# Kernel tuning notes

Hardware: AMD Instinct MI355X
Metric: run time of the kernel (lower is better)

## Reference

```python
import jax, jax.numpy as jnp
import numpy as np


def setup_inputs() -> dict:
    key = jax.random.key(0)
    k1, k2 = jax.random.split(key)
    B, C, H, W = 32, 8, 256, 256
    inp = jax.random.normal(k1, (B, C, H, W), dtype=jnp.float32)
    tgt = jax.random.uniform(k2, (B, C, H, W), dtype=jnp.float32)
    return {"input": inp, "target": tgt}


def reference(input, target):
    B, C, H, W = input.shape
    # normalized coordinate grids: (index+1)/size, as in the original loops
    x_grid = (jnp.arange(W, dtype=input.dtype) + 1.0) / W          # [W]
    y_grid = (jnp.arange(H, dtype=input.dtype) + 1.0) / H          # [H]

    # per-(b,c) softmax over the flattened heatmap (DSNT)
    p = jax.nn.softmax(input.reshape(B, C, H * W), axis=-1).reshape(B, C, H, W)
    pred_x = jnp.einsum('bchw,w->bc', p, x_grid)                   # [B, C]
    pred_y = jnp.einsum('bchw,h->bc', p, y_grid)                   # [B, C]

    # ground-truth coords from argmax of target heatmap
    idx = jnp.argmax(target.reshape(B, C, H * W), axis=-1)         # [B, C] int
    true_x = ((idx % W) + 1).astype(input.dtype) / W
    true_y = ((idx // W) + 1).astype(input.dtype) / H

    ed = jnp.sqrt((true_x - pred_x) ** 2 + (true_y - pred_y) ** 2)  # [B, C]
    # original sums over all (batch, channel) pairs, divides by batch size only
    return jnp.sum(ed) / B
```

## Files before the change

### kernel.cpp

```cpp
#include <hip/hip_runtime.h>
#include <math.h>


constexpr int HW    = 256 * 256;
constexpr int BLOCK = 256;
constexpr int SPLIT = 16;
constexpr int CHUNK4 = (HW / 4) / SPLIT;
constexpr int ITERS  = CHUNK4 / BLOCK;

typedef float vfloat4 __attribute__((ext_vector_type(4)));

__global__ __launch_bounds__(BLOCK, 8) void dsnt_partial_kernel(
        const float* __restrict__ input,
        const float* __restrict__ target,
        unsigned long long* __restrict__ ws_pk,
        float* __restrict__ ws_s,
        float* __restrict__ ws_sx,
        float* __restrict__ ws_sy)
{
    const int bc    = blockIdx.x >> 4;
    const int chunk = blockIdx.x & (SPLIT - 1);
    const int tid   = threadIdx.x;

    const vfloat4* __restrict__ in4 =
        reinterpret_cast<const vfloat4*>(input) + (size_t)bc * (HW / 4) + chunk * CHUNK4;
    const vfloat4* __restrict__ tg4 =
        reinterpret_cast<const vfloat4*>(target) + (size_t)bc * (HW / 4) + chunk * CHUNK4;

    float s = 0.f, sx = 0.f, sy = 0.f;
    float bv = -INFINITY;
    int   bi = 0x7FFFFFFF;

    const int fbase = 4 * chunk * CHUNK4;

    #pragma unroll
    for (int i = 0; i < ITERS; ++i) {
        const int j = tid + i * BLOCK;
        const vfloat4 v = __builtin_nontemporal_load(in4 + j);
        const vfloat4 t = tg4[j];
        const int f = fbase + 4 * j;
        const float y  = (float)((f >> 8) + 1) * (1.0f / 256.0f);
        const float x0 = (float)((f & 255) + 1) * (1.0f / 256.0f);

        const float e0 = __expf(v.x);
        const float e1 = __expf(v.y);
        const float e2 = __expf(v.z);
        const float e3 = __expf(v.w);
        const float es = (e0 + e1) + (e2 + e3);
        s  += es;
        sy += es * y;
        sx += e0 * x0
            + e1 * (x0 + 1.0f / 256.0f)
            + e2 * (x0 + 2.0f / 256.0f)
            + e3 * (x0 + 3.0f / 256.0f);

        if (t.x > bv) { bv = t.x; bi = f; }
        if (t.y > bv) { bv = t.y; bi = f + 1; }
        if (t.z > bv) { bv = t.z; bi = f + 2; }
        if (t.w > bv) { bv = t.w; bi = f + 3; }
    }

    unsigned long long pk =
        ((unsigned long long)__float_as_uint(bv) << 32) |
        (unsigned long long)(0xFFFFFFFFu - (unsigned)bi);

    #pragma unroll
    for (int off = 32; off > 0; off >>= 1) {
        s  += __shfl_down(s, off);
        sx += __shfl_down(sx, off);
        sy += __shfl_down(sy, off);
        const unsigned long long opk = __shfl_down(pk, off);
        pk = (opk > pk) ? opk : pk;
    }

    __shared__ float ls[4], lsx[4], lsy[4];
    __shared__ unsigned long long lpk[4];
    const int wave = tid >> 6;
    const int lane = tid & 63;
    if (lane == 0) {
        ls[wave]  = s;
        lsx[wave] = sx;
        lsy[wave] = sy;
        lpk[wave] = pk;
    }
    __syncthreads();

    if (tid == 0) {
        #pragma unroll
        for (int wv = 1; wv < 4; ++wv) {
            s  += ls[wv];
            sx += lsx[wv];
            sy += lsy[wv];
            pk = (lpk[wv] > pk) ? lpk[wv] : pk;
        }
        const int slot = blockIdx.x;
        ws_s[slot]  = s;
        ws_sx[slot] = sx;
        ws_sy[slot] = sy;
        ws_pk[slot] = pk;
    }
}

__global__ __launch_bounds__(256) void dsnt_final_kernel(
        const unsigned long long* __restrict__ ws_pk,
        const float* __restrict__ ws_s,
        const float* __restrict__ ws_sx,
        const float* __restrict__ ws_sy,
        float* __restrict__ out,
        int nmap)
{
    const int bc = threadIdx.x;
    float ed = 0.f;
    if (bc < nmap) {
        float s = 0.f, sx = 0.f, sy = 0.f;
        unsigned long long pk = 0ull;
        #pragma unroll
        for (int c = 0; c < SPLIT; ++c) {
            const int slot = bc * SPLIT + c;
            s  += ws_s[slot];
            sx += ws_sx[slot];
            sy += ws_sy[slot];
            const unsigned long long p = ws_pk[slot];
            pk = (p > pk) ? p : pk;
        }
        const unsigned bi = 0xFFFFFFFFu - (unsigned)(pk & 0xFFFFFFFFull);
        const float px = sx / s;
        const float py = sy / s;
        const float tx = (float)((bi & 255) + 1) * (1.0f / 256.0f);
        const float ty = (float)((bi >> 8) + 1) * (1.0f / 256.0f);
        const float dx = tx - px;
        const float dy = ty - py;
        ed = sqrtf(dx * dx + dy * dy);
    }

    #pragma unroll
    for (int off = 32; off > 0; off >>= 1)
        ed += __shfl_down(ed, off);

    __shared__ float led[4];
    const int wave = threadIdx.x >> 6;
    const int lane = threadIdx.x & 63;
    if (lane == 0) led[wave] = ed;
    __syncthreads();

    if (threadIdx.x == 0) {
        const float total = (led[0] + led[1]) + (led[2] + led[3]);
        out[0] = total * (1.0f / 32.0f);
    }
}

extern "C" void kernel_launch(void* const* d_in, const int* in_sizes, int n_in,
                              void* d_out, int out_size, void* d_ws, size_t ws_size,
                              hipStream_t stream) {
    const float* input  = (const float*)d_in[0];
    const float* target = (const float*)d_in[1];
    float* out = (float*)d_out;

    const int n_maps = in_sizes[0] / HW;
    const int nslot  = n_maps * SPLIT;

    unsigned long long* ws_pk = (unsigned long long*)d_ws;
    float* ws_s  = (float*)((char*)d_ws + (size_t)8  * nslot);
    float* ws_sx = (float*)((char*)d_ws + (size_t)12 * nslot);
    float* ws_sy = (float*)((char*)d_ws + (size_t)16 * nslot);

    dsnt_partial_kernel<<<nslot, BLOCK, 0, stream>>>(input, target,
                                                     ws_pk, ws_s, ws_sx, ws_sy);
    dsnt_final_kernel<<<1, 256, 0, stream>>>(ws_pk, ws_s, ws_sx, ws_sy,
                                             out, n_maps);
}
```

Baseline: 130.7 us.

## Fuse final reduction into partial kernel via last-block atomic counter

Removes the separate single-block finalize kernel. Each block increments a per-map atomic counter after writing its partials. The last block for a map combines the 16 partials, computes the Euclidean distance and atomically adds it to the output. Two memset launches are added to reset the counters and the output, so the launch count is not actually reduced. Float atomic accumulation also makes the summation order nondeterministic.

```diff
diff --git a/kernel.cpp b/kernel.cpp
--- a/kernel.cpp
+++ b/kernel.cpp
@@ -10,13 +10,15 @@
 
 typedef float vfloat4 __attribute__((ext_vector_type(4)));
 
-__global__ __launch_bounds__(BLOCK, 8) void dsnt_partial_kernel(
+__global__ __launch_bounds__(BLOCK, 8) void dsnt_fused_kernel(
         const float* __restrict__ input,
         const float* __restrict__ target,
         unsigned long long* __restrict__ ws_pk,
         float* __restrict__ ws_s,
         float* __restrict__ ws_sx,
-        float* __restrict__ ws_sy)
+        float* __restrict__ ws_sy,
+        int* __restrict__ cnt,
+        float* __restrict__ out)
 {
     const int bc    = blockIdx.x >> 4;
     const int chunk = blockIdx.x & (SPLIT - 1);
@@ -75,6 +77,7 @@
 
     __shared__ float ls[4], lsx[4], lsy[4];
     __shared__ unsigned long long lpk[4];
+    __shared__ int isLast;
     const int wave = tid >> 6;
     const int lane = tid & 63;
     if (lane == 0) {
@@ -98,54 +101,43 @@
         ws_sx[slot] = sx;
         ws_sy[slot] = sy;
         ws_pk[slot] = pk;
+        __threadfence();
+        const int old = atomicAdd(&cnt[bc], 1);
+        isLast = (old == SPLIT - 1);
     }
-}
-
-__global__ __launch_bounds__(256) void dsnt_final_kernel(
-        const unsigned long long* __restrict__ ws_pk,
-        const float* __restrict__ ws_s,
-        const float* __restrict__ ws_sx,
-        const float* __restrict__ ws_sy,
-        float* __restrict__ out,
-        int nmap)
-{
-    const int bc = threadIdx.x;
-    float ed = 0.f;
-    if (bc < nmap) {
-        float s = 0.f, sx = 0.f, sy = 0.f;
-        unsigned long long pk = 0ull;
-        #pragma unroll
-        for (int c = 0; c < SPLIT; ++c) {
-            const int slot = bc * SPLIT + c;
-            s  += ws_s[slot];
-            sx += ws_sx[slot];
-            sy += ws_sy[slot];
-            const unsigned long long p = ws_pk[slot];
-            pk = (p > pk) ? p : pk;
-        }
-        const unsigned bi = 0xFFFFFFFFu - (unsigned)(pk & 0xFFFFFFFFull);
-        const float px = sx / s;
-        const float py = sy / s;
-        const float tx = (float)((bi & 255) + 1) * (1.0f / 256.0f);
-        const float ty = (float)((bi >> 8) + 1) * (1.0f / 256.0f);
-        const float dx = tx - px;
-        const float dy = ty - py;
-        ed = sqrtf(dx * dx + dy * dy);
-    }
-
-    #pragma unroll
-    for (int off = 32; off > 0; off >>= 1)
-        ed += __shfl_down(ed, off);
-
-    __shared__ float led[4];
-    const int wave = threadIdx.x >> 6;
-    const int lane = threadIdx.x & 63;
-    if (lane == 0) led[wave] = ed;
     __syncthreads();
 
-    if (threadIdx.x == 0) {
-        const float total = (led[0] + led[1]) + (led[2] + led[3]);
-        out[0] = total * (1.0f / 32.0f);
+    if (isLast && tid < SPLIT) {
+        const int slot = bc * SPLIT + tid;
+        volatile const float* vws_s  = ws_s;
+        volatile const float* vws_sx = ws_sx;
+        volatile const float* vws_sy = ws_sy;
+        volatile const unsigned long long* vws_pk = ws_pk;
+        float fs  = vws_s[slot];
+        float fsx = vws_sx[slot];
+        float fsy = vws_sy[slot];
+        unsigned long long fpk = vws_pk[slot];
+
+        #pragma unroll
+        for (int off = 8; off > 0; off >>= 1) {
+            fs  += __shfl_down(fs, off);
+            fsx += __shfl_down(fsx, off);
+            fsy += __shfl_down(fsy, off);
+            const unsigned long long opk = __shfl_down(fpk, off);
+            fpk = (opk > fpk) ? opk : fpk;
+        }
+
+        if (tid == 0) {
+            const unsigned fbi = 0xFFFFFFFFu - (unsigned)(fpk & 0xFFFFFFFFull);
+            const float px = fsx / fs;
+            const float py = fsy / fs;
+            const float tx = (float)((fbi & 255) + 1) * (1.0f / 256.0f);
+            const float ty = (float)((fbi >> 8) + 1) * (1.0f / 256.0f);
+            const float dx = tx - px;
+            const float dy = ty - py;
+            const float ed = sqrtf(dx * dx + dy * dy);
+            atomicAdd(out, ed * (1.0f / 32.0f));
+        }
     }
 }
 
@@ -163,9 +155,11 @@
     float* ws_s  = (float*)((char*)d_ws + (size_t)8  * nslot);
     float* ws_sx = (float*)((char*)d_ws + (size_t)12 * nslot);
     float* ws_sy = (float*)((char*)d_ws + (size_t)16 * nslot);
+    int*   cnt   = (int*)  ((char*)d_ws + (size_t)20 * nslot);
 
-    dsnt_partial_kernel<<<nslot, BLOCK, 0, stream>>>(input, target,
-                                                     ws_pk, ws_s, ws_sx, ws_sy);
-    dsnt_final_kernel<<<1, 256, 0, stream>>>(ws_pk, ws_s, ws_sx, ws_sy,
-                                             out, n_maps);
+    hipMemsetAsync(cnt, 0, n_maps * sizeof(int), stream);
+    hipMemsetAsync(out, 0, sizeof(float), stream);
+    dsnt_fused_kernel<<<nslot, BLOCK, 0, stream>>>(input, target,
+                                                   ws_pk, ws_s, ws_sx, ws_sy,
+                                                   cnt, out);
 }
```

Result: slower. 309.3 us (+136.6%).
